# Optimization experiments

Measured on AMD Instinct MI355X. Metric: run time of the kernel, lower is better.

Reference implementation:

```python
import jax, jax.numpy as jnp
import numpy as np

B, L, C = 32, 1024, 32     # batch, seq_len, enc_in
D = 512                     # d_model / hidden_size
SEG = 16                    # seg_len
K = 25                      # moving_avg kernel
SX = L // SEG               # seg_num_x = 64 sequential GRU steps
PRED = 16                   # pred_len == seg_len -> seg_num_y = 1


def setup_inputs() -> dict:
    key = jax.random.key(0)
    ks = jax.random.split(key, 20)
    r = lambda i, shape: jax.random.normal(ks[i], shape, dtype=jnp.float32) * 0.05
    return {
        "x": jax.random.normal(ks[0], (B, L, C), dtype=jnp.float32),
        "W_emb": r(1, (D, SEG)), "b_emb": r(2, (D,)),
        "Wih_s": r(3, (3 * D, D)), "Whh_s": r(4, (3 * D, D)),
        "bih_s": r(5, (3 * D,)), "bhh_s": r(6, (3 * D,)),
        "Wih_t": r(7, (3 * D, D)), "Whh_t": r(8, (3 * D, D)),
        "bih_t": r(9, (3 * D,)), "bhh_t": r(10, (3 * D,)),
        "pos_s": r(11, (1, D // 2)), "ch_s": r(12, (C, D // 2)),
        "pos_t": r(13, (1, D // 2)), "ch_t": r(14, (C, D // 2)),
        "Wps": r(15, (SEG, D)), "bps": r(16, (SEG,)),
        "Wpt": r(17, (SEG, D)), "bpt": r(18, (SEG,)),
    }


def _moving_mean(x, k):
    # Autoformer moving_avg over dim 1 with edge replication (length preserved, k odd)
    pad = (k - 1) // 2
    xp = jnp.concatenate([jnp.repeat(x[:, :1], pad, 1), x, jnp.repeat(x[:, -1:], pad, 1)], axis=1)
    cs = jnp.cumsum(xp, axis=1)
    cs = jnp.concatenate([jnp.zeros_like(cs[:, :1]), cs], axis=1)
    return (cs[:, k:] - cs[:, :-k]) / k


def _gru_cell(x, h, Wih, Whh, bih, bhh):
    gi = x @ Wih.T + bih
    gh = h @ Whh.T + bhh
    ir, iz, in_ = jnp.split(gi, 3, axis=-1)
    hr, hz, hn = jnp.split(gh, 3, axis=-1)
    r = jax.nn.sigmoid(ir + hr)
    z = jax.nn.sigmoid(iz + hz)
    n = jnp.tanh(in_ + r * hn)
    return (1.0 - z) * n + z * h


def _forward(x, W_emb, b_emb, Wih_s, Whh_s, bih_s, bhh_s, Wih_t, Whh_t, bih_t, bhh_t,
             pos_s, ch_s, pos_t, ch_t, Wps, bps, Wpt, bpt):
    seq_last = jax.lax.stop_gradient(x[:, -1:, :])          # (B,1,C), detached
    xc = (x - seq_last).transpose(0, 2, 1)                  # (B,C,L)
    mean = _moving_mean(xc, K)                              # trend
    xs = xc - mean                                          # seasonal residual
    xt = mean
    # value embedding: (B*C, SX, SEG) -> (B*C, SX, D), ReLU
    xs = jax.nn.relu(xs.reshape(-1, SX, SEG) @ W_emb.T + b_emb)
    xt = jax.nn.relu(xt.reshape(-1, SX, SEG) @ W_emb.T + b_emb)
    N = B * C
    h0 = jnp.zeros((N, D), x.dtype)

    def step(carry, inp):
        hs, ht = carry
        xs_i, xt_i = inp
        hs = _gru_cell(xs_i, hs, Wih_s, Whh_s, bih_s, bhh_s)
        ht = _gru_cell(xt_i, ht, Wih_t, Whh_t, bih_t, bhh_t)
        return (hs, ht), None

    (hs, ht), _ = jax.lax.scan(step, (h0, h0), (xs.transpose(1, 0, 2), xt.transpose(1, 0, 2)))

    # decoder (seg_num_y == 1): pos/channel embedding -> one more GRUCell step
    pe_s = jnp.tile(jnp.concatenate([jnp.broadcast_to(pos_s, (C, D // 2)), ch_s], -1), (B, 1))  # (B*C,D)
    pe_t = jnp.tile(jnp.concatenate([jnp.broadcast_to(pos_t, (C, D // 2)), ch_t], -1), (B, 1))
    hs2 = _gru_cell(pe_s, hs, Wih_s, Whh_s, bih_s, bhh_s)
    ht2 = _gru_cell(pe_t, ht, Wih_t, Whh_t, bih_t, bhh_t)
    # predict heads (dropout is identity in eval)
    y = ht2 @ Wpt.T + bpt + hs2 @ Wps.T + bps               # (B*C, SEG)
    y = y.reshape(B, C, PRED).transpose(0, 2, 1)            # (B, PRED, C)
    return y + seq_last


def reference(x, W_emb, b_emb, Wih_s, Whh_s, bih_s, bhh_s, Wih_t, Whh_t, bih_t, bhh_t,
              pos_s, ch_s, pos_t, ch_t, Wps, bps, Wpt, bpt):
    return _forward(x, W_emb, b_emb, Wih_s, Whh_s, bih_s, bhh_s, Wih_t, Whh_t, bih_t, bhh_t,
                    pos_s, ch_s, pos_t, ch_t, Wps, bps, Wpt, bpt)
```

## Files before the change

kernel.cpp:

```cpp
#include <hip/hip_runtime.h>
#include <math.h>

#define B_   32
#define L_   1024
#define C_   32
#define D_   512
#define SEG_ 16
#define SX_  64
#define N_   1024

typedef _Float16 f16x8 __attribute__((ext_vector_type(8)));
typedef _Float16 f16x4 __attribute__((ext_vector_type(4)));
typedef float    f32x4 __attribute__((ext_vector_type(4)));

__device__ __forceinline__ void stage16(const void* g, void* l) {
    __builtin_amdgcn_global_load_lds((const __attribute__((address_space(1))) void*)g,
                                     (__attribute__((address_space(3))) void*)l, 16, 0, 0);
}
__device__ __forceinline__ void stage16l(const void* g, void* l) {
    __builtin_amdgcn_global_load_lds((const __attribute__((address_space(1))) void*)g,
                                     (__attribute__((address_space(3))) void*)l, 16, 0, 1);
}
__device__ __forceinline__ void store_v4_sc0(void* p, f16x8 v) {
    asm volatile("global_store_dwordx4 %0, %1, off sc0" :: "v"(p), "v"(v) : "memory");
}
__device__ __forceinline__ float fsig(float x) {
    return __builtin_amdgcn_rcpf(1.f + __expf(-x));
}
__device__ __forceinline__ float ftanh(float x) {
    return 1.f - 2.f * __builtin_amdgcn_rcpf(1.f + __expf(2.f * x));
}

__global__ __launch_bounds__(256) void setup_kernel(
    const float* __restrict__ x, float* __restrict__ xs_seg, float* __restrict__ xt_seg,
    const float* __restrict__ Wih_s, const float* __restrict__ Wih_t,
    _Float16* __restrict__ wih_pk,
    const float* __restrict__ Whh_s, const float* __restrict__ Whh_t,
    _Float16* __restrict__ whh_pk5,
    const float* __restrict__ pos_s, const float* __restrict__ ch_s,
    const float* __restrict__ pos_t, const float* __restrict__ ch_t,
    _Float16* __restrict__ pe) {
    int bid = blockIdx.x, tid = threadIdx.x;
    if (bid < 6144) {
        int e = bid * 256 + tid;
        int kk = e & 31;
        int t = e >> 5;
        int gc = t % 1536;
        int t2 = t / 1536;
        int kt = t2 & 15, gru = t2 >> 4;
        int member = gc / 192, r = gc % 192;
        int wn = r / 48, r2 = r % 48;
        int gate = r2 >> 4, jl = r2 & 15;
        int j = member * 64 + wn * 16 + jl;
        int k = kt * 32 + kk;
        const float* W = gru ? Wih_t : Wih_s;
        wih_pk[e] = (_Float16)W[(size_t)(gate * 512 + j) * 512 + k];
    } else if (bid < 12288) {
        int e = (bid - 6144) * 256 + tid;
        int fi = e & 7;
        int t = e >> 3;
        int c = t % 3072;
        int t2 = t / 3072;
        int kt = t2 & 3;
        int t3 = t2 >> 2;
        int member = t3 & 7, gru = t3 >> 3;
        int gc = c >> 4, s = c & 15;
        int q = s ^ (gc & 15);
        int k = kt * 128 + q * 8 + fi;
        int wn = gc / 48, r2 = gc % 48;
        int gate = r2 >> 4, jl = r2 & 15;
        int j = member * 64 + wn * 16 + jl;
        const float* W = gru ? Whh_t : Whh_s;
        whh_pk5[e] = (_Float16)W[(size_t)(gate * 512 + j) * 512 + k];
    } else if (bid < 16384) {
        int e = (bid - 12288) * 256 + tid;
        int k = e & 511;
        int n = (e >> 9) & 1023;
        int gru = e >> 19;
        int c = n & 31;
        const float* pos = gru ? pos_t : pos_s;
        const float* ch  = gru ? ch_t  : ch_s;
        float v = (k < 256) ? pos[k] : ch[c * 256 + (k - 256)];
        pe[e] = (_Float16)v;
    } else {
        int b2 = bid - 16384;
        int b = b2 >> 2;
        int t = ((b2 & 3) << 8) + tid;
        const float* xb    = x + (size_t)b * (L_ * C_);
        const float* xrow  = xb + (size_t)t * C_;
        const float* xlast = xb + (size_t)(L_ - 1) * C_;
        float diff[C_];
#pragma unroll
        for (int c = 0; c < C_; ++c) diff[c] = xrow[c] - xlast[c];
        float ps[C_ + 1];
        ps[0] = 0.f;
#pragma unroll
        for (int c = 0; c < C_; ++c) ps[c + 1] = ps[c] + diff[c];
        int s = t >> 4, q = t & 15;
#pragma unroll
        for (int c = 0; c < C_; ++c) {
            int lo = c - 12, hi = c + 12;
            float sum = ps[(hi < 31 ? hi : 31) + 1] - ps[lo > 0 ? lo : 0];
            if (lo < 0)  sum += (float)(-lo)     * diff[0];
            if (hi > 31) sum += (float)(hi - 31) * diff[31];
            float mean = sum * (1.0f / 25.0f);
            size_t idx = ((size_t)s * N_ + (size_t)(b * C_ + c)) * SEG_ + q;
            xt_seg[idx] = mean;
            xs_seg[idx] = diff[c] - mean;
        }
    }
}

__global__ __launch_bounds__(256) void emb_kernel(
    const float* __restrict__ xs_seg, const float* __restrict__ xt_seg,
    const float* __restrict__ W_emb, const float* __restrict__ b_emb,
    _Float16* __restrict__ emb_buf, int s0) {
    int bid = blockIdx.x;
    int gru = bid >> 8, sl = (bid >> 4) & 15, nch = bid & 15;
    int step = s0 + sl, n0 = nch * 64;
    const float* xseg = gru ? xt_seg : xs_seg;
    __shared__ float xl[64 * 16];
    int tid = threadIdx.x;
    const float* src = xseg + ((size_t)step * N_ + n0) * SEG_;
    for (int i = tid; i < 1024; i += 256) xl[i] = src[i];

    int kg = tid & 127;
    int rh = tid >> 7;
    float w[4][16], bb[4];
#pragma unroll
    for (int i = 0; i < 4; ++i) {
        int k = kg * 4 + i;
        const float4* wr = (const float4*)(W_emb + (size_t)k * 16);
#pragma unroll
        for (int v = 0; v < 4; ++v) {
            float4 tt = wr[v];
            w[i][v * 4 + 0] = tt.x; w[i][v * 4 + 1] = tt.y;
            w[i][v * 4 + 2] = tt.z; w[i][v * 4 + 3] = tt.w;
        }
        bb[i] = b_emb[k];
    }
    __syncthreads();
    _Float16* dst = emb_buf + ((size_t)(sl * 2 + gru) * N_ + n0) * D_ + kg * 4;
    for (int r = 0; r < 32; ++r) {
        int row = rh * 32 + r;
        float a0 = bb[0], a1 = bb[1], a2 = bb[2], a3 = bb[3];
#pragma unroll
        for (int q = 0; q < 16; ++q) {
            float xv = xl[row * 16 + q];
            a0 = fmaf(xv, w[0][q], a0);
            a1 = fmaf(xv, w[1][q], a1);
            a2 = fmaf(xv, w[2][q], a2);
            a3 = fmaf(xv, w[3][q], a3);
        }
        f16x4 v;
        v[0] = (_Float16)(a0 > 0.f ? a0 : 0.f);
        v[1] = (_Float16)(a1 > 0.f ? a1 : 0.f);
        v[2] = (_Float16)(a2 > 0.f ? a2 : 0.f);
        v[3] = (_Float16)(a3 > 0.f ? a3 : 0.f);
        *(f16x4*)(dst + (size_t)row * D_) = v;
    }
}

__global__ __launch_bounds__(512, 2) void gi_gemm_kernel(
    const _Float16* __restrict__ emb, const _Float16* __restrict__ pe,
    const _Float16* __restrict__ wih_pack,
    _Float16* __restrict__ gi, _Float16* __restrict__ gi_pe, int mode) {
    __shared__ __align__(16) char smem[53248];
    char* sA = smem;
    char* sB = smem + 8192;
    int Mt = blockIdx.x & 7, Nt = blockIdx.x >> 3;
    int sl = blockIdx.y, gru = blockIdx.z;
    int tid = threadIdx.x, w = tid >> 6, lane = tid & 63;
    int wm = w & 1, wn = w >> 1, ml = lane & 15, qq = lane >> 4;

    const char* Ab = mode ? (const char*)(pe  + (size_t)gru * N_ * D_)
                          : (const char*)(emb + (size_t)(sl * 2 + gru) * N_ * D_);
    const char* Bb = (const char*)wih_pack + (size_t)gru * 16 * 1536 * 64
                     + (size_t)Nt * 192 * 64;

    int rA = tid >> 2, kqA = (tid & 3) ^ ((rA >> 1) & 3);
    const char* gA = Ab + (size_t)(Mt * 128 + rA) * 1024 + kqA * 16;
    int g1 = tid >> 2, kq1 = (tid & 3) ^ ((g1 >> 1) & 3);
    int c2 = 512 + tid, g2 = c2 >> 2, kq2 = (c2 & 3) ^ ((g2 >> 1) & 3);

    int offA[4], offB[3];
#pragma unroll
    for (int mf = 0; mf < 4; ++mf) {
        int row = wm * 64 + mf * 16 + ml;
        offA[mf] = (row * 4 + (qq ^ ((row >> 1) & 3))) * 16;
    }
#pragma unroll
    for (int g = 0; g < 3; ++g) {
        int gc = wn * 48 + g * 16 + ml;
        offB[g] = (gc * 4 + (qq ^ ((gc >> 1) & 3))) * 16;
    }

    f32x4 acc[4][3];
#pragma unroll
    for (int mf = 0; mf < 4; ++mf)
#pragma unroll
        for (int g = 0; g < 3; ++g) {
            f32x4 z = {0.f, 0.f, 0.f, 0.f};
            acc[mf][g] = z;
        }

    for (int kt = 0; kt < 16; ++kt) {
        __syncthreads();
        stage16(gA + kt * 64, sA + w * 1024);
        const char* Bkt = Bb + (size_t)kt * (1536 * 64);
        stage16(Bkt + g1 * 64 + kq1 * 16, sB + w * 1024);
        if (w < 4) stage16(Bkt + g2 * 64 + kq2 * 16, sB + 8192 + w * 1024);
        asm volatile("s_waitcnt vmcnt(0)" ::: "memory");
        __syncthreads();
        f16x8 a[4];
#pragma unroll
        for (int mf = 0; mf < 4; ++mf) a[mf] = *(const f16x8*)(sA + offA[mf]);
#pragma unroll
        for (int g = 0; g < 3; ++g) {
            f16x8 b = *(const f16x8*)(sB + offB[g]);
#pragma unroll
            for (int mf = 0; mf < 4; ++mf)
                acc[mf][g] = __builtin_amdgcn_mfma_f32_16x16x32_f16(a[mf], b, acc[mf][g], 0, 0, 0);
        }
    }

    __syncthreads();
#pragma unroll
    for (int mf = 0; mf < 4; ++mf) {
        int wm_c = mf >> 1, rt = mf & 1;
        int tid_c = (wn * 2 + wm_c) * 64 + qq * 16 + ml;
        char* base = smem + wm * 26624 + tid_c * 52;
#pragma unroll
        for (int g = 0; g < 3; ++g)
#pragma unroll
            for (int reg = 0; reg < 4; ++reg) {
                int v = rt * 12 + reg * 3 + g;
                *(_Float16*)(base + v * 2) = (_Float16)acc[mf][g][reg];
            }
    }
    __syncthreads();
    _Float16* ob = mode ? gi_pe + (size_t)gru * 8 * 16 * 512 * 24
                        : gi    + (size_t)(sl * 2 + gru) * 8 * 16 * 512 * 24;
    char* obB = (char*)ob;
#pragma unroll
    for (int s = 0; s < 6; ++s) {
        int o = tid * 16 + s * 8192;
        int mc = o / 24576;
        int o2 = o - mc * 24576;
        int tc = o2 / 48;
        int r  = o2 - tc * 48;
        const char* src = smem + mc * 26624 + tc * 52 + r;
        int4 val;
        val.x = *(const int*)(src);
        val.y = *(const int*)(src + 4);
        val.z = *(const int*)(src + 8);
        val.w = *(const int*)(src + 12);
        *(int4*)(obB + (size_t)(Nt * 16 + Mt * 2 + mc) * 24576 + o2) = val;
    }
}

__global__ __launch_bounds__(512) void gru_chain_kernel(
    const _Float16* __restrict__ whh_pk5,
    const _Float16* __restrict__ gi_base,
    const float* __restrict__ bih_s, const float* __restrict__ bhh_s,
    const float* __restrict__ bih_t, const float* __restrict__ bhh_t,
    _Float16* __restrict__ hbf0, _Float16* __restrict__ hbf1,
    unsigned* __restrict__ flags, int nsteps, int sbase) {
    __shared__ __align__(16) char sA[65536];
    __shared__ __align__(16) char sEx[49152];
    int bid = blockIdx.x;
    int member = bid >> 5, chain = bid & 31;
    int Mt = chain & 15, gru = chain >> 4;
    int tid = threadIdx.x, w = tid >> 6, lane = tid & 63;
    int ml = lane & 15, qq = lane >> 4;
    int km = w & 1, wn = w >> 1;

    const char* h0 = (const char*)hbf0 + ((size_t)gru * N_ + Mt * 64) * 1024;
    const char* h1 = (const char*)hbf1 + ((size_t)gru * N_ + Mt * 64) * 1024;

    f16x8 bfr[3][8];
    {
        const _Float16* Wb = whh_pk5 + (size_t)(gru * 8 + member) * 4 * 24576;
#pragma unroll
        for (int g = 0; g < 3; ++g) {
            int gc = wn * 48 + g * 16 + ml;
#pragma unroll
            for (int ks = 0; ks < 8; ++ks) {
                int kt = km * 2 + (ks >> 2);
                int q8 = ((ks & 3) * 4 + qq) ^ (gc & 15);
                bfr[g][ks] = *(const f16x8*)(Wb + (size_t)kt * 24576
                                             + (size_t)(gc * 16 + q8) * 8);
            }
        }
    }

    int cS0 = (lane & 48) | ((lane & 15) ^ (w & 15));
    int cS1 = (lane & 48) | ((lane & 15) ^ ((w + 8) & 15));

    int offR[4], cp[8];
#pragma unroll
    for (int rt = 0; rt < 4; ++rt) offR[rt] = (rt * 16 + ml) * 1024;
#pragma unroll
    for (int ks = 0; ks < 8; ++ks) {
        int c = km * 32 + ks * 4 + qq;
        cp[ks] = ((c & 48) | ((c & 15) ^ ml)) * 16;
    }

    const float* bi = gru ? bih_t : bih_s;
    const float* bh = gru ? bhh_t : bhh_s;
    int j = member * 64 + wn * 16 + ml;
    float bir = bi[j], biz = bi[D_ + j], bin = bi[2 * D_ + j];
    float bhr = bh[j], bhz = bh[D_ + j], bhn = bh[2 * D_ + j];
    float hp[2][4];
#pragma unroll
    for (int rtL = 0; rtL < 2; ++rtL)
#pragma unroll
        for (int reg = 0; reg < 4; ++reg) {
            int row = Mt * 64 + km * 32 + rtL * 16 + qq * 4 + reg;
            hp[rtL][reg] = (float)hbf0[((size_t)gru * N_ + row) * D_ + j];
        }

    unsigned* fbase = flags + chain * 256;
    const _Float16* giTid0 = gi_base
        + (((size_t)gru * 8 + member) * 16 + Mt) * 512 * 24 + (size_t)tid * 24;
    size_t giStep = (size_t)2 * 8 * 16 * 512 * 24;

    int dir0 = sbase & 1;
    f16x8 gv0, gv1, gv2;
    {
        const _Float16* gp = giTid0;
        gv0 = *(const f16x8*)(gp);
        gv1 = *(const f16x8*)(gp + 8);
        gv2 = *(const f16x8*)(gp + 16);
        const char* hin = dir0 ? h1 : h0;
#pragma unroll
        for (int r = 0; r < 8; ++r) {
            int row = r * 8 + w;
            stage16l(hin + (size_t)row * 1024 + (size_t)((r & 1) ? cS1 : cS0) * 16,
                     sA + row * 1024);
        }
    }

    for (int it = 0; it < nsteps; ++it) {
        int gstep = sbase + it;
        _Float16* hout = (gstep & 1) ? hbf0 : hbf1;

        f32x4 acc[4][3];
#pragma unroll
        for (int rt = 0; rt < 4; ++rt)
#pragma unroll
            for (int g = 0; g < 3; ++g) {
                f32x4 z = {0.f, 0.f, 0.f, 0.f};
                acc[rt][g] = z;
            }

        asm volatile("s_waitcnt vmcnt(0)" ::: "memory");
        __syncthreads();

        int itn = (it + 1 < nsteps) ? it + 1 : it;
        const _Float16* gpn = giTid0 + (size_t)itn * giStep;
        f16x8 ngv0 = *(const f16x8*)(gpn);
        f16x8 ngv1 = *(const f16x8*)(gpn + 8);
        f16x8 ngv2 = *(const f16x8*)(gpn + 16);
        __builtin_amdgcn_sched_barrier(0);

#pragma unroll
        for (int ks = 0; ks < 8; ++ks) {
            f16x8 a0 = *(const f16x8*)(sA + offR[0] + cp[ks]);
            f16x8 a1 = *(const f16x8*)(sA + offR[1] + cp[ks]);
            f16x8 a2 = *(const f16x8*)(sA + offR[2] + cp[ks]);
            f16x8 a3 = *(const f16x8*)(sA + offR[3] + cp[ks]);
#pragma unroll
            for (int g = 0; g < 3; ++g) {
                acc[0][g] = __builtin_amdgcn_mfma_f32_16x16x32_f16(a0, bfr[g][ks], acc[0][g], 0, 0, 0);
                acc[1][g] = __builtin_amdgcn_mfma_f32_16x16x32_f16(a1, bfr[g][ks], acc[1][g], 0, 0, 0);
                acc[2][g] = __builtin_amdgcn_mfma_f32_16x16x32_f16(a2, bfr[g][ks], acc[2][g], 0, 0, 0);
                acc[3][g] = __builtin_amdgcn_mfma_f32_16x16x32_f16(a3, bfr[g][ks], acc[3][g], 0, 0, 0);
            }
        }

        char* exw = sEx + (size_t)(wn * 64 + lane) * 16;
        if (km == 0) {
#pragma unroll
            for (int g = 0; g < 3; ++g) {
                *(f32x4*)(exw + (size_t)(6 + g) * 4096) = acc[2][g];
                *(f32x4*)(exw + (size_t)(9 + g) * 4096) = acc[3][g];
            }
        } else {
#pragma unroll
            for (int g = 0; g < 3; ++g) {
                *(f32x4*)(exw + (size_t)(0 + g) * 4096) = acc[0][g];
                *(f32x4*)(exw + (size_t)(3 + g) * 4096) = acc[1][g];
            }
        }
        __syncthreads();
        f32x4 s0[3], s1[3];
        if (km == 0) {
#pragma unroll
            for (int g = 0; g < 3; ++g) {
                s0[g] = acc[0][g] + *(const f32x4*)(exw + (size_t)(0 + g) * 4096);
                s1[g] = acc[1][g] + *(const f32x4*)(exw + (size_t)(3 + g) * 4096);
            }
        } else {
#pragma unroll
            for (int g = 0; g < 3; ++g) {
                s0[g] = acc[2][g] + *(const f32x4*)(exw + (size_t)(6 + g) * 4096);
                s1[g] = acc[3][g] + *(const f32x4*)(exw + (size_t)(9 + g) * 4096);
            }
        }

        char* sH = sA;
        int colb = (wn * 16 + ml) * 2;
#pragma unroll
        for (int reg = 0; reg < 4; ++reg) {
            int v0 = reg * 3;
            float gr = (float)((v0 + 0) < 8 ? gv0[(v0 + 0) & 7]
                      : ((v0 + 0) < 16 ? gv1[(v0 + 0) & 7] : gv2[(v0 + 0) & 7]));
            float gz = (float)((v0 + 1) < 8 ? gv0[(v0 + 1) & 7]
                      : ((v0 + 1) < 16 ? gv1[(v0 + 1) & 7] : gv2[(v0 + 1) & 7]));
            float gn = (float)((v0 + 2) < 8 ? gv0[(v0 + 2) & 7]
                      : ((v0 + 2) < 16 ? gv1[(v0 + 2) & 7] : gv2[(v0 + 2) & 7]));
            float r = fsig(s0[0][reg] + gr + bir + bhr);
            float z = fsig(s0[1][reg] + gz + biz + bhz);
            float nn = ftanh(gn + bin + r * (s0[2][reg] + bhn));
            float hv = (1.f - z) * nn + z * hp[0][reg];
            hp[0][reg] = hv;
            int rl = km * 32 + qq * 4 + reg;
            *(_Float16*)(sH + rl * 144 + colb) = (_Float16)hv;
        }
#pragma unroll
        for (int reg = 0; reg < 4; ++reg) {
            int v0 = 12 + reg * 3;
            float gr = (float)((v0 + 0) < 8 ? gv0[(v0 + 0) & 7]
                      : ((v0 + 0) < 16 ? gv1[(v0 + 0) & 7] : gv2[(v0 + 0) & 7]));
            float gz = (float)((v0 + 1) < 8 ? gv0[(v0 + 1) & 7]
                      : ((v0 + 1) < 16 ? gv1[(v0 + 1) & 7] : gv2[(v0 + 1) & 7]));
            float gn = (float)((v0 + 2) < 8 ? gv0[(v0 + 2) & 7]
                      : ((v0 + 2) < 16 ? gv1[(v0 + 2) & 7] : gv2[(v0 + 2) & 7]));
            float r = fsig(s1[0][reg] + gr + bir + bhr);
            float z = fsig(s1[1][reg] + gz + biz + bhz);
            float nn = ftanh(gn + bin + r * (s1[2][reg] + bhn));
            float hv = (1.f - z) * nn + z * hp[1][reg];
            hp[1][reg] = hv;
            int rl = km * 32 + 16 + qq * 4 + reg;
            *(_Float16*)(sH + rl * 144 + colb) = (_Float16)hv;
        }
        __syncthreads();
        {
            int srow = tid >> 3, spart = tid & 7;
            f16x8 hv8 = *(const f16x8*)(sH + srow * 144 + spart * 16);
            _Float16* gdst = hout + ((size_t)gru * N_ + Mt * 64 + srow) * D_
                             + member * 64 + spart * 8;
            store_v4_sc0(gdst, hv8);
        }

        asm volatile("s_waitcnt vmcnt(0)" ::: "memory");
        __syncthreads();
        if (tid == 0)
            __hip_atomic_store(fbase + member * 32, (unsigned)(gstep + 1),
                               __ATOMIC_RELAXED, __HIP_MEMORY_SCOPE_AGENT);

        if (it < nsteps - 1) {
            if (w == 0) {
                const unsigned* fp = fbase + (lane & 7) * 32;
                unsigned tgt = (unsigned)(gstep + 1);
                int guard = 0;
                while (true) {
                    unsigned v = __hip_atomic_load(fp, __ATOMIC_RELAXED,
                                                   __HIP_MEMORY_SCOPE_AGENT);
                    if (__all(v >= tgt)) break;
                    __builtin_amdgcn_s_sleep(1);
                    if (++guard > (1 << 20)) break;
                }
            }
            __syncthreads();
            const char* hinN = ((gstep + 1) & 1) ? h1 : h0;
#pragma unroll
            for (int r = 0; r < 8; ++r) {
                int row = r * 8 + w;
                stage16l(hinN + (size_t)row * 1024 + (size_t)((r & 1) ? cS1 : cS0) * 16,
                         sA + row * 1024);
            }
        }
        gv0 = ngv0; gv1 = ngv1; gv2 = ngv2;
    }
}

__global__ __launch_bounds__(256) void head_kernel(
    const _Float16* __restrict__ hs2, const _Float16* __restrict__ ht2,
    const float* __restrict__ Wps, const float* __restrict__ bps,
    const float* __restrict__ Wpt, const float* __restrict__ bpt,
    const float* __restrict__ x, float* __restrict__ out) {
    int g = blockIdx.x * 256 + threadIdx.x;
    int n = g >> 4, p = g & 15;
    int b = n >> 5, c = n & 31;
    const _Float16* hs = hs2 + (size_t)n * D_;
    const _Float16* ht = ht2 + (size_t)n * D_;
    const float* ws = Wps + (size_t)p * D_;
    const float* wt = Wpt + (size_t)p * D_;
    float acc = bps[p] + bpt[p];
    for (int k = 0; k < D_; ++k)
        acc += (float)hs[k] * ws[k] + (float)ht[k] * wt[k];
    float last = x[((size_t)b * L_ + (L_ - 1)) * C_ + c];
    out[((size_t)b * SEG_ + p) * C_ + c] = acc + last;
}

extern "C" void kernel_launch(void* const* d_in, const int* in_sizes, int n_in,
                              void* d_out, int out_size, void* d_ws, size_t ws_size,
                              hipStream_t stream) {
    const float* x     = (const float*)d_in[0];
    const float* W_emb = (const float*)d_in[1];
    const float* b_emb = (const float*)d_in[2];
    const float* Wih_s = (const float*)d_in[3];
    const float* Whh_s = (const float*)d_in[4];
    const float* bih_s = (const float*)d_in[5];
    const float* bhh_s = (const float*)d_in[6];
    const float* Wih_t = (const float*)d_in[7];
    const float* Whh_t = (const float*)d_in[8];
    const float* bih_t = (const float*)d_in[9];
    const float* bhh_t = (const float*)d_in[10];
    const float* pos_s = (const float*)d_in[11];
    const float* ch_s  = (const float*)d_in[12];
    const float* pos_t = (const float*)d_in[13];
    const float* ch_t  = (const float*)d_in[14];
    const float* Wps   = (const float*)d_in[15];
    const float* bps   = (const float*)d_in[16];
    const float* Wpt   = (const float*)d_in[17];
    const float* bpt   = (const float*)d_in[18];
    float* out = (float*)d_out;

    const size_t SZ_XS    = (size_t)SX_ * N_ * SEG_ * 4;
    const size_t SZ_EMB   = (size_t)16 * 2 * N_ * D_ * 2;
    const size_t SZ_GIB   = (size_t)16 * 2 * 8 * 16 * 512 * 24 * 2;
    const size_t SZ_GIPE  = (size_t)2 * 8 * 16 * 512 * 24 * 2;
    const size_t SZ_PE    = (size_t)2 * N_ * D_ * 2;
    const size_t SZ_WIH   = (size_t)2 * 16 * 1536 * 32 * 2;
    const size_t SZ_WHH   = (size_t)2 * 8 * 4 * 3072 * 8 * 2;
    const size_t SZ_H     = (size_t)2 * N_ * D_ * 2;
    const size_t SZ_FLAGS = 32 * 256 * 4;
    const size_t fixed = 2 * SZ_XS + SZ_EMB + SZ_GIPE + SZ_PE + SZ_WIH + SZ_WHH
                         + 2 * SZ_H + SZ_FLAGS;
    const bool big2 = ws_size >= fixed + 2 * SZ_GIB;
    const size_t gi_bytes = big2 ? 2 * SZ_GIB : SZ_GIB;

    char* p = (char*)d_ws;
    float* xs_seg = (float*)p;          p += SZ_XS;
    float* xt_seg = (float*)p;          p += SZ_XS;
    _Float16* emb_buf = (_Float16*)p;   p += SZ_EMB;
    _Float16* gi_buf  = (_Float16*)p;   p += gi_bytes;
    _Float16* gi_pe   = (_Float16*)p;   p += SZ_GIPE;
    _Float16* pe_buf  = (_Float16*)p;   p += SZ_PE;
    _Float16* wih_pk  = (_Float16*)p;   p += SZ_WIH;
    _Float16* whh_pk5 = (_Float16*)p;   p += SZ_WHH;
    _Float16* hbf0 = (_Float16*)p;      p += SZ_H;
    _Float16* hbf1 = (_Float16*)p;      p += SZ_H;
    unsigned* flags = (unsigned*)p;     p += SZ_FLAGS;

    hipMemsetAsync(hbf0, 0, SZ_H, stream);
    hipMemsetAsync(flags, 0, SZ_FLAGS, stream);

    setup_kernel<<<16512, 256, 0, stream>>>(
        x, xs_seg, xt_seg, Wih_s, Wih_t, wih_pk, Whh_s, Whh_t, whh_pk5,
        pos_s, ch_s, pos_t, ch_t, pe_buf);

    const size_t giBatchElems = (size_t)16 * 2 * 8 * 16 * 512 * 24;
    if (big2) {
        for (int b = 0; b < 2; ++b) {
            emb_kernel<<<512, 256, 0, stream>>>(xs_seg, xt_seg, W_emb, b_emb,
                                                emb_buf, b * 16);
            gi_gemm_kernel<<<dim3(64, 16, 2), 512, 0, stream>>>(
                emb_buf, pe_buf, wih_pk, gi_buf + (size_t)b * giBatchElems, gi_pe, 0);
        }
        gru_chain_kernel<<<256, 512, 0, stream>>>(
            whh_pk5, gi_buf, bih_s, bhh_s, bih_t, bhh_t,
            hbf0, hbf1, flags, 32, 0);
        for (int b = 2; b < 4; ++b) {
            emb_kernel<<<512, 256, 0, stream>>>(xs_seg, xt_seg, W_emb, b_emb,
                                                emb_buf, b * 16);
            gi_gemm_kernel<<<dim3(64, 16, 2), 512, 0, stream>>>(
                emb_buf, pe_buf, wih_pk, gi_buf + (size_t)(b - 2) * giBatchElems,
                gi_pe, 0);
        }
        gi_gemm_kernel<<<dim3(64, 1, 2), 512, 0, stream>>>(
            emb_buf, pe_buf, wih_pk, gi_buf, gi_pe, 1);
        gru_chain_kernel<<<256, 512, 0, stream>>>(
            whh_pk5, gi_buf, bih_s, bhh_s, bih_t, bhh_t,
            hbf0, hbf1, flags, 33, 32);
    } else {
        for (int b = 0; b < 4; ++b) {
            emb_kernel<<<512, 256, 0, stream>>>(xs_seg, xt_seg, W_emb, b_emb,
                                                emb_buf, b * 16);
            gi_gemm_kernel<<<dim3(64, 16, 2), 512, 0, stream>>>(
                emb_buf, pe_buf, wih_pk, gi_buf, gi_pe, 0);
            gru_chain_kernel<<<256, 512, 0, stream>>>(
                whh_pk5, gi_buf, bih_s, bhh_s, bih_t, bhh_t,
                hbf0, hbf1, flags, 16, b * 16);
        }
        gi_gemm_kernel<<<dim3(64, 1, 2), 512, 0, stream>>>(
            emb_buf, pe_buf, wih_pk, gi_buf, gi_pe, 1);
        gru_chain_kernel<<<256, 512, 0, stream>>>(
            whh_pk5, gi_pe, bih_s, bhh_s, bih_t, bhh_t,
            hbf0, hbf1, flags, 1, 64);
    }

    head_kernel<<<N_ * SEG_ / 256, 256, 0, stream>>>(
        hbf1, hbf1 + (size_t)N_ * D_, Wps, bps, Wpt, bpt, x, out);
}
```

Before: 751.8 us.

## Triple-buffer GI GEMM LDS staging and use per-wave step flags in recurrence

The input-gate GEMM now stages tiles into three rotating LDS buffers and prefetches the next K-tile before computing the current one. This replaces the load, wait-all, compute sequence and needs only one barrier per iteration instead of two. The persistent GRU recurrence kernel drops the block-wide barrier before signalling. Each wave now publishes its own flag slot, and the poller waits on all 64 wave flags. This cuts sync latency on the serial critical path, in exchange for more LDS use (which may cut occupancy) and a larger flag array.

```diff
diff --git a/kernel.cpp b/kernel.cpp
--- a/kernel.cpp
+++ b/kernel.cpp
@@ -165,9 +165,9 @@
     const _Float16* __restrict__ emb, const _Float16* __restrict__ pe,
     const _Float16* __restrict__ wih_pack,
     _Float16* __restrict__ gi, _Float16* __restrict__ gi_pe, int mode) {
-    __shared__ __align__(16) char smem[53248];
-    char* sA = smem;
-    char* sB = smem + 8192;
+    __shared__ __align__(16) char smem[61440];
+    char* bufA[3] = { smem, smem + 8192, smem + 16384 };
+    char* bufB[3] = { smem + 24576, smem + 36864, smem + 49152 };
     int Mt = blockIdx.x & 7, Nt = blockIdx.x >> 3;
     int sl = blockIdx.y, gru = blockIdx.z;
     int tid = threadIdx.x, w = tid >> 6, lane = tid & 63;
@@ -204,20 +204,38 @@
             acc[mf][g] = z;
         }
 
+    {
+        stage16(gA, bufA[0] + w * 1024);
+        const char* Bkt = Bb;
+        stage16(Bkt + g1 * 64 + kq1 * 16, bufB[0] + w * 1024);
+        if (w < 4) stage16(Bkt + g2 * 64 + kq2 * 16, bufB[0] + 8192 + w * 1024);
+    }
+
+#pragma unroll
     for (int kt = 0; kt < 16; ++kt) {
+        if (kt < 15) {
+            int kn = kt + 1;
+            stage16(gA + kn * 64, bufA[kn % 3] + w * 1024);
+            const char* Bkt = Bb + (size_t)kn * (1536 * 64);
+            stage16(Bkt + g1 * 64 + kq1 * 16, bufB[kn % 3] + w * 1024);
+            if (w < 4) {
+                stage16(Bkt + g2 * 64 + kq2 * 16, bufB[kn % 3] + 8192 + w * 1024);
+                asm volatile("s_waitcnt vmcnt(3)" ::: "memory");
+            } else {
+                asm volatile("s_waitcnt vmcnt(2)" ::: "memory");
+            }
+        } else {
+            asm volatile("s_waitcnt vmcnt(0)" ::: "memory");
+        }
         __syncthreads();
-        stage16(gA + kt * 64, sA + w * 1024);
-        const char* Bkt = Bb + (size_t)kt * (1536 * 64);
-        stage16(Bkt + g1 * 64 + kq1 * 16, sB + w * 1024);
-        if (w < 4) stage16(Bkt + g2 * 64 + kq2 * 16, sB + 8192 + w * 1024);
-        asm volatile("s_waitcnt vmcnt(0)" ::: "memory");
-        __syncthreads();
+        const char* cA = bufA[kt % 3];
+        const char* cB = bufB[kt % 3];
         f16x8 a[4];
 #pragma unroll
-        for (int mf = 0; mf < 4; ++mf) a[mf] = *(const f16x8*)(sA + offA[mf]);
+        for (int mf = 0; mf < 4; ++mf) a[mf] = *(const f16x8*)(cA + offA[mf]);
 #pragma unroll
         for (int g = 0; g < 3; ++g) {
-            f16x8 b = *(const f16x8*)(sB + offB[g]);
+            f16x8 b = *(const f16x8*)(cB + offB[g]);
 #pragma unroll
             for (int mf = 0; mf < 4; ++mf)
                 acc[mf][g] = __builtin_amdgcn_mfma_f32_16x16x32_f16(a[mf], b, acc[mf][g], 0, 0, 0);
@@ -320,7 +338,7 @@
             hp[rtL][reg] = (float)hbf0[((size_t)gru * N_ + row) * D_ + j];
         }
 
-    unsigned* fbase = flags + chain * 256;
+    unsigned* fbase = flags + (size_t)chain * 2048;
     const _Float16* giTid0 = gi_base
         + (((size_t)gru * 8 + member) * 16 + Mt) * 512 * 24 + (size_t)tid * 24;
     size_t giStep = (size_t)2 * 8 * 16 * 512 * 24;
@@ -455,14 +473,13 @@
         }
 
         asm volatile("s_waitcnt vmcnt(0)" ::: "memory");
-        __syncthreads();
-        if (tid == 0)
-            __hip_atomic_store(fbase + member * 32, (unsigned)(gstep + 1),
+        if (lane == 0)
+            __hip_atomic_store(fbase + (member * 8 + w) * 32, (unsigned)(gstep + 1),
                                __ATOMIC_RELAXED, __HIP_MEMORY_SCOPE_AGENT);
 
         if (it < nsteps - 1) {
             if (w == 0) {
-                const unsigned* fp = fbase + (lane & 7) * 32;
+                const unsigned* fp = fbase + (size_t)lane * 32;
                 unsigned tgt = (unsigned)(gstep + 1);
                 int guard = 0;
                 while (true) {
@@ -537,7 +554,7 @@
     const size_t SZ_WIH   = (size_t)2 * 16 * 1536 * 32 * 2;
     const size_t SZ_WHH   = (size_t)2 * 8 * 4 * 3072 * 8 * 2;
     const size_t SZ_H     = (size_t)2 * N_ * D_ * 2;
-    const size_t SZ_FLAGS = 32 * 256 * 4;
+    const size_t SZ_FLAGS = (size_t)32 * 2048 * 4;
     const size_t fixed = 2 * SZ_XS + SZ_EMB + SZ_GIPE + SZ_PE + SZ_WIH + SZ_WHH
                          + 2 * SZ_H + SZ_FLAGS;
     const bool big2 = ws_size >= fixed + 2 * SZ_GIB;
```

After: 787.6 us. 1.05x slower.
